# Kernel optimization log

Measured on AMD Instinct MI355X. Metric: run time of the kernel, lower is better.

The kernel has to match this reference:

```python
import jax, jax.numpy as jnp
import numpy as np

BUF = 16  # max polygon vertex buffer (convex 9-gon clipped by 4 half-planes -> <= 13 verts)


def _shoelace(V, c):
    # area of polygon stored in buffer V[:c]
    i = jnp.arange(V.shape[0])
    nxt = jnp.where(i + 1 < c, i + 1, 0)
    Vn = V[nxt]
    contrib = jnp.where(i < c, V[:, 0] * Vn[:, 1] - Vn[:, 0] * V[:, 1], 0.0)
    return 0.5 * jnp.abs(contrib.sum())


def _convex_hull(P):
    # exact convex hull of n small points; returns CCW-ordered vertex buffer [BUF,2] and count
    n = P.shape[0]
    d = P[None, :, :] - P[:, None, :]  # p_j - p_i
    minc = jnp.full((n, n), jnp.inf, P.dtype)
    for k in range(n):  # fixed small loop, keeps memory at [n,n]
        w = (P[k] - P)[:, None, :]
        minc = jnp.minimum(minc, d[..., 0] * w[..., 1] - d[..., 1] * w[..., 0])
    minc = jax.lax.stop_gradient(minc)  # hull membership is discrete
    edge = (minc >= -1e-6) & (~jnp.eye(n, dtype=bool))  # (i,j) is CCW hull edge iff all pts left
    hull = edge.any(1)
    cnt = hull.sum()
    cen = (P * hull[:, None]).sum(0) / jnp.maximum(cnt, 1)
    ang = jnp.arctan2(P[:, 1] - cen[1], P[:, 0] - cen[0])
    keyv = jnp.where(hull, jax.lax.stop_gradient(ang), jnp.inf)
    order = jnp.argsort(keyv)
    V = jnp.zeros((BUF, 2), P.dtype).at[:n].set(P[order])
    return V, cnt


def _clip(V, c, a, b):
    # Sutherland-Hodgman clip of convex polygon (V,c) by half-plane left of a->b
    i = jnp.arange(BUF)
    active = i < c
    nxt = jnp.where(i + 1 < c, i + 1, 0)
    nx = V[nxt]
    e = b - a
    s_cur = e[0] * (V[:, 1] - a[1]) - e[1] * (V[:, 0] - a[0])
    s_nxt = e[0] * (nx[:, 1] - a[1]) - e[1] * (nx[:, 0] - a[0])
    in_cur = s_cur >= 0
    in_nxt = s_nxt >= 0
    den = s_cur - s_nxt
    safe = jnp.abs(den) > 1e-9
    t = jnp.where(safe, s_cur / jnp.where(safe, den, 1.0), 0.0)
    ipt = V + t[:, None] * (nx - V)
    f_int = active & (in_cur != in_nxt)
    f_nxt = active & in_nxt
    pts = jnp.stack([ipt, nx], 1).reshape(2 * BUF, 2)
    flg = jnp.stack([f_int, f_nxt], 1).reshape(2 * BUF)
    pos = jnp.cumsum(flg) - 1
    idx = jnp.where(flg, pos, BUF)  # invalid slots dropped
    out = jnp.zeros((BUF, 2), V.dtype).at[idx].set(pts, mode='drop')
    return out, flg.sum()


def _order_ccw(Q):
    cen = Q.mean(0)
    ang = jnp.arctan2(Q[:, 1] - cen[1], Q[:, 0] - cen[0])
    return Q[jnp.argsort(jax.lax.stop_gradient(ang))]


def _per_point(gt4, p9):
    # giou_loss + out_of_box loss for one (gt quad, 9 pred points) pair
    gt = _order_ccw(gt4)
    Vp, cp = _convex_hull(p9)          # predicted convex polygon (OrientedRepPoints convex hull)
    a_pred = _shoelace(Vp, cp)
    a_gt = _shoelace(jnp.zeros((BUF, 2), gt.dtype).at[:4].set(gt), 4)
    V, c = Vp, cp
    for e in range(4):
        V, c = _clip(V, c, gt[e], gt[(e + 1) % 4])
    a_int = _shoelace(V, c)
    union = a_pred + a_gt - a_int
    iou = a_int / (union + 1e-16)
    Vh, ch = _convex_hull(jnp.concatenate([gt4, p9], 0))  # hull of all 13 points
    a_hull = _shoelace(Vh, ch)
    giou = iou - (a_hull - union) / (a_hull + 1e-16)
    # out-of-box distance: positive distance of pred points outside the gt quad edges
    b = jnp.roll(gt, -1, 0)
    e2 = b - gt
    rel = p9[:, None, :] - gt[None, :, :]
    s = (e2[None, :, 0] * rel[..., 1] - e2[None, :, 1] * rel[..., 0]) / (jnp.linalg.norm(e2, axis=1)[None, :] + 1e-9)
    oob = jax.nn.relu((-s).max(1)).mean()
    return 1.0 - giou, oob


def _assign(points_xy, points_lvl, gt_obb):
    # OBBPointAssigner: sequential per-GT closest-point assignment (pos_num=1, scale=4)
    xs = gt_obb[:, 0::2]
    ys = gt_obb[:, 1::2]
    xmin, xmax = xs.min(1), xs.max(1)
    ymin, ymax = ys.min(1), ys.max(1)
    cxy = jnp.stack([(xmin + xmax) / 2, (ymin + ymax) / 2], 1)
    wh = jnp.maximum(jnp.stack([xmax - xmin, ymax - ymin], 1), 1e-6)
    lvl_min, lvl_max = points_lvl.min(), points_lvl.max()
    glvl = jnp.clip(((jnp.log2(wh[:, 0] / 4.0) + jnp.log2(wh[:, 1] / 4.0)) / 2).astype(jnp.int32), lvl_min, lvl_max)
    K = gt_obb.shape[0]
    Np = points_xy.shape[0]

    def body(carry, g):
        inds, dist = carry
        c_xy, c_wh, c_lvl, gi = g
        dmask = points_lvl == c_lvl
        dd = jnp.linalg.norm((points_xy - c_xy) / c_wh, axis=1)
        dd = jnp.where(dmask, dd, jnp.inf)
        j = jnp.argmin(dd)
        md = dd[j]
        better = md < dist[j]
        inds = inds.at[j].set(jnp.where(better, gi + 1, inds[j]))
        dist = dist.at[j].set(jnp.where(better, md, dist[j]))
        return (inds, dist), None

    init = (jnp.zeros(Np, jnp.int32), jnp.full(Np, jnp.inf, points_xy.dtype))
    (inds, _), _ = jax.lax.scan(body, init, (cxy, wh, glvl, jnp.arange(K, dtype=jnp.int32)))
    return inds


def _stage(rep, inds, labels, gt_obb):
    posm = (labels > 0).astype(rep.dtype)
    gidx = jnp.maximum(inds - 1, 0)
    gt4 = gt_obb[gidx].reshape(-1, 4, 2)
    p9 = rep.reshape(-1, 9, 2)
    gl, oob = jax.vmap(_per_point)(gt4, p9)
    npos = jnp.maximum(posm.sum(), 1.0)
    return (gl * posm).sum() / npos, (oob * posm).sum() / npos


def _forward(rpi, rpr, cls, stride, gob, glab):
    stride = jax.lax.stop_gradient(stride)
    plvl = jnp.log2(stride).astype(jnp.int32)
    inds_i = _assign(jax.lax.stop_gradient(rpi[:, 8:10]), plvl, jax.lax.stop_gradient(gob))
    inds_r = _assign(jax.lax.stop_gradient(rpr[:, 8:10]), plvl, jax.lax.stop_gradient(gob))
    lab_i = jnp.where(inds_i > 0, glab[jnp.maximum(inds_i - 1, 0)], 0)
    lab_r = jnp.where(inds_r > 0, glab[jnp.maximum(inds_r - 1, 0)], 0)
    loc_i, sc_i = _stage(rpi, inds_i, lab_i, gob)
    loc_r, sc_r = _stage(rpr, inds_r, lab_r, gob)
    logp = jax.nn.log_softmax(cls, -1)
    cls_loss = -jnp.take_along_axis(logp, lab_r[:, None], 1).mean()
    return 1.0 * cls_loss + 0.3 * loc_i + 1.0 * loc_r + 0.05 * sc_i + 0.1 * sc_r


def setup_inputs() -> dict:
    key = jax.random.key(0)
    ks = jax.random.split(key, 8)
    strides = [8, 16, 32, 64, 128]
    batch = 2
    centers_list, stride_list = [], []
    for s in strides:
        hw = 1536 // s
        c = (jnp.arange(hw, dtype=jnp.float32) + 0.5) * s
        gx, gy = jnp.meshgrid(c, c, indexing='ij')
        cen = jnp.stack([gx.reshape(-1), gy.reshape(-1)], 1)
        cen = jnp.tile(cen, (batch, 1))
        centers_list.append(cen)
        stride_list.append(jnp.full((cen.shape[0],), float(s), jnp.float32))
    centers = jnp.concatenate(centers_list, 0)
    points_stride = jnp.concatenate(stride_list, 0)
    N = centers.shape[0]  # 98208
    base = jnp.tile(centers[:, None, :], (1, 9, 1)).reshape(N, 18)
    scale18 = jnp.repeat(points_stride[:, None], 18, 1)
    rpi = base + jax.random.normal(ks[0], (N, 18), jnp.float32) * scale18 * 1.5
    rpr = base + jax.random.normal(ks[1], (N, 18), jnp.float32) * scale18 * 1.0
    classification = jax.random.normal(ks[2], (N, 16), jnp.float32)
    K = 64
    cx = jax.random.uniform(ks[3], (K,), minval=128.0, maxval=1408.0)
    cy = jax.random.uniform(ks[4], (K,), minval=128.0, maxval=1408.0)
    w = jax.random.uniform(ks[5], (K,), minval=48.0, maxval=400.0)
    h = jax.random.uniform(ks[6], (K,), minval=48.0, maxval=400.0)
    th = jax.random.uniform(ks[7], (K,), minval=0.0, maxval=float(np.pi))
    ct, st = jnp.cos(th), jnp.sin(th)
    dx = jnp.stack([-w, w, w, -w], 1) / 2
    dy = jnp.stack([-h, -h, h, h], 1) / 2
    xs = cx[:, None] + dx * ct[:, None] - dy * st[:, None]
    ys = cy[:, None] + dx * st[:, None] + dy * ct[:, None]
    gt_obboxes = jnp.stack([xs, ys], 2).reshape(K, 8)
    gt_labels = jax.random.randint(jax.random.fold_in(key, 7), (K,), 1, 16)
    return {"rep_points_init": rpi, "rep_points_refine": rpr, "classification": classification,
            "points_stride": points_stride, "gt_obboxes": gt_obboxes, "gt_labels": gt_labels}


def reference(rep_points_init, rep_points_refine, classification, points_stride, gt_obboxes, gt_labels):
    return _forward(rep_points_init, rep_points_refine, classification, points_stride, gt_obboxes, gt_labels)
```

## Files before the change

kernel.cpp:

```cpp
#include <hip/hip_runtime.h>
#include <math.h>
#include <stdint.h>

#pragma clang fp contract(off)

#define SUB 16

struct WS {
  double sums[8];
  unsigned long long packed[128];
  int lo[8], hi[8];
  float gcx[64], gcy[64], gw[64], gh[64];
  int glvl[64];
  unsigned cntpub[2];
  unsigned done2;
};

__global__ void k_pre(const float* __restrict__ stridev, const float* __restrict__ gob,
                      int N, int K, WS* ws) {
  __shared__ int bnd[9];
  __shared__ int slmin, slmax;
  int t = threadIdx.x;
  if (t < 8) ws->sums[t] = 0.0;
  if (t < 128) ws->packed[t] = ~0ULL;
  if (t == 0) { ws->done2 = 0u; ws->cntpub[0] = 0u; ws->cntpub[1] = 0u; }
  if (t < 9) {
    float v = (float)(1 << t);
    int lo = 0, hi = N;
    while (lo < hi) { int mid = (lo + hi) >> 1; if (stridev[mid] < v) lo = mid + 1; else hi = mid; }
    bnd[t] = lo;
  }
  __syncthreads();
  if (t == 0) {
    int a = 7, b = 0;
    for (int l = 0; l < 8; l++) {
      int lo = bnd[l], hi = bnd[l + 1];
      ws->lo[l] = lo; ws->hi[l] = hi;
      if (hi > lo) { if (l < a) a = l; if (l > b) b = l; }
    }
    slmin = a; slmax = b;
  }
  __syncthreads();
  if (t < K && t < 64) {
    const float* g = gob + t * 8;
    float x0 = g[0], x1 = g[2], x2 = g[4], x3 = g[6];
    float y0 = g[1], y1 = g[3], y2 = g[5], y3 = g[7];
    float xmin = fminf(fminf(x0, x1), fminf(x2, x3));
    float xmax = fmaxf(fmaxf(x0, x1), fmaxf(x2, x3));
    float ymin = fminf(fminf(y0, y1), fminf(y2, y3));
    float ymax = fmaxf(fmaxf(y0, y1), fmaxf(y2, y3));
    float w = fmaxf(xmax - xmin, 1e-6f);
    float h = fmaxf(ymax - ymin, 1e-6f);
    ws->gcx[t] = (xmin + xmax) * 0.5f;
    ws->gcy[t] = (ymin + ymax) * 0.5f;
    ws->gw[t] = w; ws->gh[t] = h;
    int gl = (int)((log2f(w * 0.25f) + log2f(h * 0.25f)) * 0.5f);
    gl = gl < slmin ? slmin : (gl > slmax ? slmax : gl);
    ws->glvl[t] = gl;
  }
}

__global__ void __launch_bounds__(256) k_main(const float* __restrict__ rpi,
                                              const float* __restrict__ rpr,
                                              const float* __restrict__ cls,
                                              int N, int K, int AB, WS* ws) {
  __shared__ unsigned long long sb[256];
  int t = threadIdx.x;
  int b = blockIdx.x;
  if (b < AB) {
    int s = b % SUB;
    int ak = b / SUB;
    int a = ak / K;
    int k = ak % K;
    int L = ws->glvl[k];
    int lo = ws->lo[L], hi = ws->hi[L];
    float cx = ws->gcx[k], cy = ws->gcy[k], w = ws->gw[k], h = ws->gh[k];
    const float* rep = a ? rpr : rpi;
    unsigned long long best = ~0ULL;
    for (int i = lo + s * 256 + t; i < hi; i += SUB * 256) {
      const float2 p = *(const float2*)(rep + (size_t)i * 18 + 8);
      float dx = (p.x - cx) / w, dy = (p.y - cy) / h;
      float dd = sqrtf(dx * dx + dy * dy);
      unsigned long long pk = ((unsigned long long)__float_as_uint(dd) << 32) | (unsigned)i;
      if (pk < best) best = pk;
    }
    sb[t] = best;
    __syncthreads();
    for (int off = 128; off > 0; off >>= 1) {
      if (t < off) { unsigned long long o = sb[t + off]; if (o < sb[t]) sb[t] = o; }
      __syncthreads();
    }
    if (t == 0) atomicMin(&ws->packed[a * 64 + k], sb[0]);
  } else {
    int i = (b - AB) * 256 + t;
    double v = 0.0;
    if (i < N) {
      const float4* r = (const float4*)(cls + (size_t)i * 16);
      float4 q0 = r[0], q1 = r[1], q2 = r[2], q3 = r[3];
      float x[16] = {q0.x, q0.y, q0.z, q0.w, q1.x, q1.y, q1.z, q1.w,
                     q2.x, q2.y, q2.z, q2.w, q3.x, q3.y, q3.z, q3.w};
      float m = x[0];
      for (int j = 1; j < 16; j++) m = fmaxf(m, x[j]);
      float ssum = 0.f;
      for (int j = 0; j < 16; j++) ssum += expf(x[j] - m);
      v = (double)(logf(ssum) + m - x[0]);
    }
    double* sd = (double*)sb;
    sd[t] = v;
    __syncthreads();
    for (int off = 128; off > 0; off >>= 1) {
      if (t < off) sd[t] += sd[t + off];
      __syncthreads();
    }
    if (t == 0) atomicAdd(&ws->sums[0], sd[0]);
  }
}


__device__ __forceinline__ float shoe(const float* VX, const float* VY, int c) {
  float s = 0.f;
  #pragma unroll
  for (int i = 0; i < 16; i++) {
    if (i < c) {
      int nx = (i + 1 < c) ? ((i + 1 < 16) ? i + 1 : 15) : 0;
      s += VX[i] * VY[nx] - VX[nx] * VY[i];
    }
  }
  return 0.5f * fabsf(s);
}

__device__ __forceinline__ int clip_edge(const float* SX, const float* SY, float* DX, float* DY,
                                         int c, float ax, float ay, float bx, float by, int lane) {
  if (lane < 16) { DX[lane] = 0.f; DY[lane] = 0.f; }
  bool f_int = false, f_nxt = false;
  float ix = 0.f, iy = 0.f, nxv = 0.f, nyv = 0.f;
  if (lane < 16 && lane < c) {
    int nxt = (lane + 1 < c) ? lane + 1 : 0;
    if (nxt > 15) nxt = 15;
    float cxv = SX[lane], cyv = SY[lane];
    nxv = SX[nxt]; nyv = SY[nxt];
    float ex = bx - ax, ey = by - ay;
    float s_cur = ex * (cyv - ay) - ey * (cxv - ax);
    float s_nxt = ex * (nyv - ay) - ey * (nxv - ax);
    bool in_cur = s_cur >= 0.f, in_nxt = s_nxt >= 0.f;
    float den = s_cur - s_nxt;
    bool safe = fabsf(den) > 1e-9f;
    float tt = safe ? s_cur / den : 0.f;
    ix = cxv + tt * (nxv - cxv);
    iy = cyv + tt * (nyv - cyv);
    f_int = (in_cur != in_nxt);
    f_nxt = in_nxt;
  }
  unsigned long long bi = __ballot(f_int), bn = __ballot(f_nxt);
  unsigned long long lt = (1ULL << lane) - 1ULL;
  int below = __popcll(bi & lt) + __popcll(bn & lt);
  if (f_int && below < 16) { DX[below] = ix; DY[below] = iy; }
  int posn = below + (f_int ? 1 : 0);
  if (f_nxt && posn < 16) { DX[posn] = nxv; DY[posn] = nyv; }
  __syncthreads();
  return __popcll(bi) + __popcll(bn);
}

template <int NP>
__device__ __forceinline__ int hull_wave(const float* PX, const float* PY, int base,
                                         float* VX, float* VY, float* KEY, int lane) {
  constexpr int TOT = NP * NP;
  unsigned long long B0 = 0, B1 = 0, B2 = 0;
  {
    bool h = false;
    int idx = lane;
    if (idx < TOT) {
      int i = idx / NP, j = idx % NP;
      if (i != j) {
        float pix = PX[base + i], piy = PY[base + i];
        float dx = PX[base + j] - pix, dy = PY[base + j] - piy;
        float m = INFINITY;
        #pragma unroll
        for (int k = 0; k < NP; k++)
          m = fminf(m, dx * (PY[base + k] - piy) - dy * (PX[base + k] - pix));
        h = (m >= -1e-6f);
      }
    }
    B0 = __ballot(h);
  }
  if constexpr (TOT > 64) {
    bool h = false;
    int idx = lane + 64;
    if (idx < TOT) {
      int i = idx / NP, j = idx % NP;
      if (i != j) {
        float pix = PX[base + i], piy = PY[base + i];
        float dx = PX[base + j] - pix, dy = PY[base + j] - piy;
        float m = INFINITY;
        #pragma unroll
        for (int k = 0; k < NP; k++)
          m = fminf(m, dx * (PY[base + k] - piy) - dy * (PX[base + k] - pix));
        h = (m >= -1e-6f);
      }
    }
    B1 = __ballot(h);
  }
  if constexpr (TOT > 128) {
    bool h = false;
    int idx = lane + 128;
    if (idx < TOT) {
      int i = idx / NP, j = idx % NP;
      if (i != j) {
        float pix = PX[base + i], piy = PY[base + i];
        float dx = PX[base + j] - pix, dy = PY[base + j] - piy;
        float m = INFINITY;
        #pragma unroll
        for (int k = 0; k < NP; k++)
          m = fminf(m, dx * (PY[base + k] - piy) - dy * (PX[base + k] - pix));
        h = (m >= -1e-6f);
      }
    }
    B2 = __ballot(h);
  }
  bool hull_i = false;
  if (lane < NP) {
    int s = lane * NP, w = s >> 6, off = s & 63;
    unsigned long long Bw = (w == 0) ? B0 : ((w == 1) ? B1 : B2);
    unsigned long long Bw1 = (w == 0) ? B1 : ((w == 1) ? B2 : 0ULL);
    unsigned long long bits = Bw >> off;
    if (off) bits |= Bw1 << (64 - off);
    hull_i = (bits & ((1ULL << NP) - 1ULL)) != 0ULL;
  }
  unsigned long long hmask = __ballot(hull_i);
  int cnt = __popcll(hmask);
  float cx = 0.f, cy = 0.f;
  #pragma unroll
  for (int k = 0; k < NP; k++)
    if ((hmask >> k) & 1ULL) { cx += PX[base + k]; cy += PY[base + k]; }
  float dn = (float)(cnt > 1 ? cnt : 1);
  cx /= dn; cy /= dn;
  if (lane < NP)
    KEY[lane] = hull_i ? atan2f(PY[base + lane] - cy, PX[base + lane] - cx) : INFINITY;
  if (lane < 16) { VX[lane] = 0.f; VY[lane] = 0.f; }
  __syncthreads();
  if (lane < NP) {
    float ki = KEY[lane];
    int r = 0;
    #pragma unroll
    for (int j2 = 0; j2 < NP; j2++) {
      float kj = KEY[j2];
      r += (int)((kj < ki) || (kj == ki && j2 < lane));
    }
    VX[r] = PX[base + lane];
    VY[r] = PY[base + lane];
  }
  __syncthreads();
  return cnt;
}

__global__ void __launch_bounds__(64) k_post(const float* __restrict__ rpi,
                                             const float* __restrict__ rpr,
                                             const float* __restrict__ gob,
                                             const int* __restrict__ glab,
                                             const float* __restrict__ cls,
                                             int N, float* out, WS* ws) {
  __shared__ float PXs[16], PYs[16], VX[16], VY[16], DX[16], DY[16], KEY[16], RED[9];
  __shared__ int SJ[64];
  __shared__ unsigned long long SMK[64];
  int lane = threadIdx.x;
  int b = blockIdx.x;
  int a = b >> 6, p = b & 63;

  unsigned long long pk = ws->packed[a * 64 + lane];
  bool valid = (pk != ~0ULL);
  SJ[lane] = valid ? (int)(unsigned)(pk & 0xffffffffu) : (-1 - lane);
  SMK[lane] = (pk & 0xffffffff00000000ULL) | (unsigned)lane;
  __syncthreads();
  bool win = false;
  if (valid) {
    int j = SJ[lane];
    unsigned long long me = SMK[lane];
    win = true;
    for (int o = 0; o < 64; o++)
      if (SJ[o] == j && SMK[o] < me) win = false;
  }
  unsigned long long wmask = __ballot(win);
  int cnt = __popcll(wmask);
  if (p == 0 && lane == 0) atomicExch(&ws->cntpub[a], (unsigned)cnt);

  bool active = (p < cnt);
  if (active) {
    int kk = 0;
    { int c2 = 0;
      for (int o = 0; o < 64; o++)
        if ((wmask >> o) & 1ULL) { if (c2 == p) { kk = o; break; } c2++; } }
    int j = SJ[kk];
    const float* rep = (a ? rpr : rpi) + (size_t)j * 18;
    const float* gt8 = gob + (size_t)kk * 8;
    if (lane < 4) { PXs[lane] = gt8[2 * lane]; PYs[lane] = gt8[2 * lane + 1]; }
    else if (lane < 13) { int q = lane - 4; PXs[lane] = rep[2 * q]; PYs[lane] = rep[2 * q + 1]; }
    __syncthreads();

    float cenx = (((PXs[0] + PXs[1]) + PXs[2]) + PXs[3]) / 4.f;
    float ceny = (((PYs[0] + PYs[1]) + PYs[2]) + PYs[3]) / 4.f;
    float angv[4];
    int r4[4];
    #pragma unroll
    for (int i = 0; i < 4; i++) angv[i] = atan2f(PYs[i] - ceny, PXs[i] - cenx);
    #pragma unroll
    for (int i = 0; i < 4; i++) {
      int r = 0;
      #pragma unroll
      for (int j2 = 0; j2 < 4; j2++)
        r += (int)((angv[j2] < angv[i]) || (angv[j2] == angv[i] && j2 < i));
      r4[i] = r;
    }
    float qx[4], qy[4];
    #pragma unroll
    for (int d = 0; d < 4; d++) {
      float sx = 0.f, sy = 0.f;
      #pragma unroll
      for (int i = 0; i < 4; i++) if (r4[i] == d) { sx = PXs[i]; sy = PYs[i]; }
      qx[d] = sx; qy[d] = sy;
    }

    int cp = hull_wave<9>(PXs, PYs, 4, VX, VY, KEY, lane);
    float a_pred = shoe(VX, VY, cp);

    float sgt = 0.f;
    #pragma unroll
    for (int i = 0; i < 4; i++) {
      int nx = (i + 1) & 3;
      sgt += qx[i] * qy[nx] - qx[nx] * qy[i];
    }
    float a_gt = 0.5f * fabsf(sgt);

    int c = cp;
    c = clip_edge(VX, VY, DX, DY, c, qx[0], qy[0], qx[1], qy[1], lane);
    c = clip_edge(DX, DY, VX, VY, c, qx[1], qy[1], qx[2], qy[2], lane);
    c = clip_edge(VX, VY, DX, DY, c, qx[2], qy[2], qx[3], qy[3], lane);
    c = clip_edge(DX, DY, VX, VY, c, qx[3], qy[3], qx[0], qy[0], lane);
    float a_int = shoe(VX, VY, c);

    float uni = a_pred + a_gt - a_int;
    float iou = a_int / (uni + 1e-16f);

    int ch = hull_wave<13>(PXs, PYs, 0, VX, VY, KEY, lane);
    float a_hull = shoe(VX, VY, ch);
    float giou = iou - (a_hull - uni) / (a_hull + 1e-16f);
    float gl = 1.f - giou;

    float mxv = -INFINITY;
    if (lane < 36) {
      int pp = lane >> 2, e = lane & 3;
      float ax = e == 0 ? qx[0] : e == 1 ? qx[1] : e == 2 ? qx[2] : qx[3];
      float ay = e == 0 ? qy[0] : e == 1 ? qy[1] : e == 2 ? qy[2] : qy[3];
      float bx2 = e == 0 ? qx[1] : e == 1 ? qx[2] : e == 2 ? qx[3] : qx[0];
      float by2 = e == 0 ? qy[1] : e == 1 ? qy[2] : e == 2 ? qy[3] : qy[0];
      float ex = bx2 - ax, ey = by2 - ay;
      float nrm = sqrtf(ex * ex + ey * ey) + 1e-9f;
      float px = PXs[4 + pp], py = PYs[4 + pp];
      float s = (ex * (py - ay) - ey * (px - ax)) / nrm;
      mxv = -s;
    }
    float o1 = __shfl_xor(mxv, 1); mxv = fmaxf(mxv, o1);
    float o2 = __shfl_xor(mxv, 2); mxv = fmaxf(mxv, o2);
    if (lane < 36 && (lane & 3) == 0) RED[lane >> 2] = fmaxf(mxv, 0.f);
    __syncthreads();
    if (lane == 0) {
      float acc = 0.f;
      #pragma unroll
      for (int pp = 0; pp < 9; pp++) acc += RED[pp];
      float oob = acc / 9.f;
      atomicAdd(&ws->sums[1 + a * 2], (double)gl);
      atomicAdd(&ws->sums[2 + a * 2], (double)oob);
      if (a == 1) {
        int lab = glab[kk];
        double corr = (double)cls[(size_t)j * 16] - (double)cls[(size_t)j * 16 + lab];
        atomicAdd(&ws->sums[0], corr);
      }
    }
  }

  __syncthreads();
  if (lane == 0) {
    __threadfence();
    unsigned d = atomicAdd(&ws->done2, 1u);
    if (d == gridDim.x - 1) {
      __threadfence();
      double s0 = atomicAdd(&ws->sums[0], 0.0);
      double s1 = atomicAdd(&ws->sums[1], 0.0);
      double s2 = atomicAdd(&ws->sums[2], 0.0);
      double s3 = atomicAdd(&ws->sums[3], 0.0);
      double s4 = atomicAdd(&ws->sums[4], 0.0);
      unsigned c0 = atomicAdd(&ws->cntpub[0], 0u);
      unsigned c1 = atomicAdd(&ws->cntpub[1], 0u);
      double n0 = (double)(c0 > 1u ? c0 : 1u);
      double n1 = (double)(c1 > 1u ? c1 : 1u);
      out[0] = (float)(s0 / (double)N + 0.3 * (s1 / n0) + 1.0 * (s3 / n1) +
                       0.05 * (s2 / n0) + 0.1 * (s4 / n1));
    }
  }
}

extern "C" void kernel_launch(void* const* d_in, const int* in_sizes, int n_in,
                              void* d_out, int out_size, void* d_ws, size_t ws_size,
                              hipStream_t stream) {
  const float* rpi = (const float*)d_in[0];
  const float* rpr = (const float*)d_in[1];
  const float* cls = (const float*)d_in[2];
  const float* pstride = (const float*)d_in[3];
  const float* gob = (const float*)d_in[4];
  const int* glab = (const int*)d_in[5];
  int N = in_sizes[3];
  int K = in_sizes[5];
  if (K > 64) K = 64;
  WS* ws = (WS*)d_ws;

  int AB = 2 * K * SUB;
  int nb = (N + 255) / 256;
  k_pre<<<1, 256, 0, stream>>>(pstride, gob, N, K, ws);
  k_main<<<AB + nb, 256, 0, stream>>>(rpi, rpr, cls, N, K, AB, ws);
  k_post<<<128, 64, 0, stream>>>(rpi, rpr, gob, glab, cls, N, (float*)d_out, ws);
}
```

Measured before the change: 107.2 us.

## Compact rep-point coordinates into workspace and move softmax loss into pre-kernel

The pre-kernel becomes a multi-block pass that copies the center (x,y) of each rep point into a contiguous float2 array in the workspace and computes per-block cross-entropy partial sums. Level boundaries are now found with a parallel scan over exponent bits instead of binary search. The nearest-point kernel reads the compacted array, so each block touches 8 bytes per point instead of strided 72-byte rows. The last post block sums the class partials instead of using many double atomics. The cost is an extra full pass writing the compact arrays and a deterministic partial-sum buffer.

After: 203.6 us. 1.9x slower.

```diff
diff --git a/kernel.cpp b/kernel.cpp
--- a/kernel.cpp
+++ b/kernel.cpp
@@ -14,106 +14,130 @@
   int glvl[64];
   unsigned cntpub[2];
   unsigned done2;
+  unsigned pad0;
+  double clsPart[1024];
 };
 
-__global__ void k_pre(const float* __restrict__ stridev, const float* __restrict__ gob,
-                      int N, int K, WS* ws) {
-  __shared__ int bnd[9];
+__device__ __forceinline__ int lvl_of(float s) {
+  return (int)(__float_as_uint(s) >> 23) - 127;
+}
+
+__global__ void __launch_bounds__(256) k_pre(const float* __restrict__ rpi,
+                                             const float* __restrict__ rpr,
+                                             const float* __restrict__ cls,
+                                             const float* __restrict__ stridev,
+                                             const float* __restrict__ gob,
+                                             int N, int K, WS* ws) {
+  __shared__ double sd[256];
   __shared__ int slmin, slmax;
   int t = threadIdx.x;
-  if (t < 8) ws->sums[t] = 0.0;
-  if (t < 128) ws->packed[t] = ~0ULL;
-  if (t == 0) { ws->done2 = 0u; ws->cntpub[0] = 0u; ws->cntpub[1] = 0u; }
-  if (t < 9) {
-    float v = (float)(1 << t);
-    int lo = 0, hi = N;
-    while (lo < hi) { int mid = (lo + hi) >> 1; if (stridev[mid] < v) lo = mid + 1; else hi = mid; }
-    bnd[t] = lo;
-  }
-  __syncthreads();
-  if (t == 0) {
-    int a = 7, b = 0;
-    for (int l = 0; l < 8; l++) {
-      int lo = bnd[l], hi = bnd[l + 1];
-      ws->lo[l] = lo; ws->hi[l] = hi;
-      if (hi > lo) { if (l < a) a = l; if (l > b) b = l; }
-    }
-    slmin = a; slmax = b;
-  }
-  __syncthreads();
-  if (t < K && t < 64) {
-    const float* g = gob + t * 8;
-    float x0 = g[0], x1 = g[2], x2 = g[4], x3 = g[6];
-    float y0 = g[1], y1 = g[3], y2 = g[5], y3 = g[7];
-    float xmin = fminf(fminf(x0, x1), fminf(x2, x3));
-    float xmax = fmaxf(fmaxf(x0, x1), fmaxf(x2, x3));
-    float ymin = fminf(fminf(y0, y1), fminf(y2, y3));
-    float ymax = fmaxf(fmaxf(y0, y1), fmaxf(y2, y3));
-    float w = fmaxf(xmax - xmin, 1e-6f);
-    float h = fmaxf(ymax - ymin, 1e-6f);
-    ws->gcx[t] = (xmin + xmax) * 0.5f;
-    ws->gcy[t] = (ymin + ymax) * 0.5f;
-    ws->gw[t] = w; ws->gh[t] = h;
-    int gl = (int)((log2f(w * 0.25f) + log2f(h * 0.25f)) * 0.5f);
-    gl = gl < slmin ? slmin : (gl > slmax ? slmax : gl);
-    ws->glvl[t] = gl;
-  }
-}
-
-__global__ void __launch_bounds__(256) k_main(const float* __restrict__ rpi,
-                                              const float* __restrict__ rpr,
-                                              const float* __restrict__ cls,
-                                              int N, int K, int AB, WS* ws) {
+  float2* xyi = (float2*)(ws + 1);
+  float2* xyr = xyi + N;
+
+  if (blockIdx.x == 0) {
+    if (t < 8) { ws->sums[t] = 0.0; ws->lo[t] = 0; ws->hi[t] = 0; }
+    if (t < 128) ws->packed[t] = ~0ULL;
+    if (t == 0) { ws->done2 = 0u; ws->cntpub[0] = 0u; ws->cntpub[1] = 0u; }
+    __syncthreads();
+    int chunk = (N + 255) >> 8;
+    int beg = t * chunk, end = beg + chunk;
+    if (end > N) end = N;
+    if (beg < N) {
+      float prev = (beg > 0) ? stridev[beg - 1] : 0.f;
+      for (int i = beg; i < end; i++) {
+        float s = stridev[i];
+        int l = lvl_of(s);
+        if ((unsigned)l < 8u) {
+          if (i == 0) {
+            ws->lo[l] = 0;
+          } else {
+            int lp = lvl_of(prev);
+            if (lp != l) { if ((unsigned)lp < 8u) ws->hi[lp] = i; ws->lo[l] = i; }
+          }
+          if (i == N - 1) ws->hi[l] = N;
+        }
+        prev = s;
+      }
+    }
+    __syncthreads();
+    if (t == 0) {
+      int a = 7, b = 0;
+      for (int l = 0; l < 8; l++)
+        if (ws->hi[l] > ws->lo[l]) { if (l < a) a = l; if (l > b) b = l; }
+      slmin = a; slmax = b;
+    }
+    __syncthreads();
+    if (t < K && t < 64) {
+      const float* g = gob + t * 8;
+      float x0 = g[0], x1 = g[2], x2 = g[4], x3 = g[6];
+      float y0 = g[1], y1 = g[3], y2 = g[5], y3 = g[7];
+      float xmin = fminf(fminf(x0, x1), fminf(x2, x3));
+      float xmax = fmaxf(fmaxf(x0, x1), fmaxf(x2, x3));
+      float ymin = fminf(fminf(y0, y1), fminf(y2, y3));
+      float ymax = fmaxf(fmaxf(y0, y1), fmaxf(y2, y3));
+      float w = fmaxf(xmax - xmin, 1e-6f);
+      float h = fmaxf(ymax - ymin, 1e-6f);
+      ws->gcx[t] = (xmin + xmax) * 0.5f;
+      ws->gcy[t] = (ymin + ymax) * 0.5f;
+      ws->gw[t] = w; ws->gh[t] = h;
+      int gl = (int)((log2f(w * 0.25f) + log2f(h * 0.25f)) * 0.5f);
+      gl = gl < slmin ? slmin : (gl > slmax ? slmax : gl);
+      ws->glvl[t] = gl;
+    }
+  }
+
+  double acc = 0.0;
+  for (int i = blockIdx.x * 256 + t; i < N; i += gridDim.x * 256) {
+    const float* pi = rpi + (size_t)i * 18;
+    const float* pr = rpr + (size_t)i * 18;
+    xyi[i] = *(const float2*)(pi + 8);
+    xyr[i] = *(const float2*)(pr + 8);
+    const float4* r = (const float4*)(cls + (size_t)i * 16);
+    float4 q0 = r[0], q1 = r[1], q2 = r[2], q3 = r[3];
+    float x[16] = {q0.x, q0.y, q0.z, q0.w, q1.x, q1.y, q1.z, q1.w,
+                   q2.x, q2.y, q2.z, q2.w, q3.x, q3.y, q3.z, q3.w};
+    float m = x[0];
+    for (int j = 1; j < 16; j++) m = fmaxf(m, x[j]);
+    float ssum = 0.f;
+    for (int j = 0; j < 16; j++) ssum += expf(x[j] - m);
+    acc += (double)(logf(ssum) + m - x[0]);
+  }
+  sd[t] = acc;
+  __syncthreads();
+  for (int off = 128; off > 0; off >>= 1) {
+    if (t < off) sd[t] += sd[t + off];
+    __syncthreads();
+  }
+  if (t == 0) ws->clsPart[blockIdx.x] = sd[0];
+}
+
+__global__ void __launch_bounds__(256) k_main(int N, int K, WS* ws) {
   __shared__ unsigned long long sb[256];
   int t = threadIdx.x;
   int b = blockIdx.x;
-  if (b < AB) {
-    int s = b % SUB;
-    int ak = b / SUB;
-    int a = ak / K;
-    int k = ak % K;
-    int L = ws->glvl[k];
-    int lo = ws->lo[L], hi = ws->hi[L];
-    float cx = ws->gcx[k], cy = ws->gcy[k], w = ws->gw[k], h = ws->gh[k];
-    const float* rep = a ? rpr : rpi;
-    unsigned long long best = ~0ULL;
-    for (int i = lo + s * 256 + t; i < hi; i += SUB * 256) {
-      const float2 p = *(const float2*)(rep + (size_t)i * 18 + 8);
-      float dx = (p.x - cx) / w, dy = (p.y - cy) / h;
-      float dd = sqrtf(dx * dx + dy * dy);
-      unsigned long long pk = ((unsigned long long)__float_as_uint(dd) << 32) | (unsigned)i;
-      if (pk < best) best = pk;
-    }
-    sb[t] = best;
-    __syncthreads();
-    for (int off = 128; off > 0; off >>= 1) {
-      if (t < off) { unsigned long long o = sb[t + off]; if (o < sb[t]) sb[t] = o; }
-      __syncthreads();
-    }
-    if (t == 0) atomicMin(&ws->packed[a * 64 + k], sb[0]);
-  } else {
-    int i = (b - AB) * 256 + t;
-    double v = 0.0;
-    if (i < N) {
-      const float4* r = (const float4*)(cls + (size_t)i * 16);
-      float4 q0 = r[0], q1 = r[1], q2 = r[2], q3 = r[3];
-      float x[16] = {q0.x, q0.y, q0.z, q0.w, q1.x, q1.y, q1.z, q1.w,
-                     q2.x, q2.y, q2.z, q2.w, q3.x, q3.y, q3.z, q3.w};
-      float m = x[0];
-      for (int j = 1; j < 16; j++) m = fmaxf(m, x[j]);
-      float ssum = 0.f;
-      for (int j = 0; j < 16; j++) ssum += expf(x[j] - m);
-      v = (double)(logf(ssum) + m - x[0]);
-    }
-    double* sd = (double*)sb;
-    sd[t] = v;
-    __syncthreads();
-    for (int off = 128; off > 0; off >>= 1) {
-      if (t < off) sd[t] += sd[t + off];
-      __syncthreads();
-    }
-    if (t == 0) atomicAdd(&ws->sums[0], sd[0]);
-  }
+  int s = b % SUB;
+  int ak = b / SUB;
+  int a = ak / K;
+  int k = ak % K;
+  int L = ws->glvl[k];
+  int lo = ws->lo[L], hi = ws->hi[L];
+  float cx = ws->gcx[k], cy = ws->gcy[k], w = ws->gw[k], h = ws->gh[k];
+  const float2* xy = (const float2*)(ws + 1) + (a ? N : 0);
+  unsigned long long best = ~0ULL;
+  for (int i = lo + s * 256 + t; i < hi; i += SUB * 256) {
+    float2 p = xy[i];
+    float dx = (p.x - cx) / w, dy = (p.y - cy) / h;
+    float dd = sqrtf(dx * dx + dy * dy);
+    unsigned long long pk = ((unsigned long long)__float_as_uint(dd) << 32) | (unsigned)i;
+    if (pk < best) best = pk;
+  }
+  sb[t] = best;
+  __syncthreads();
+  for (int off = 128; off > 0; off >>= 1) {
+    if (t < off) { unsigned long long o = sb[t + off]; if (o < sb[t]) sb[t] = o; }
+    __syncthreads();
+  }
+  if (t == 0 && sb[0] != ~0ULL) atomicMin(&ws->packed[a * 64 + k], sb[0]);
 }
 
 
@@ -258,10 +282,12 @@
                                              const float* __restrict__ gob,
                                              const int* __restrict__ glab,
                                              const float* __restrict__ cls,
-                                             int N, float* out, WS* ws) {
+                                             int N, int nbCls, float* out, WS* ws) {
   __shared__ float PXs[16], PYs[16], VX[16], VY[16], DX[16], DY[16], KEY[16], RED[9];
   __shared__ int SJ[64];
   __shared__ unsigned long long SMK[64];
+  __shared__ double SRED[64];
+  __shared__ int islast;
   int lane = threadIdx.x;
   int b = blockIdx.x;
   int a = b >> 6, p = b & 63;
@@ -381,9 +407,19 @@
   if (lane == 0) {
     __threadfence();
     unsigned d = atomicAdd(&ws->done2, 1u);
-    if (d == gridDim.x - 1) {
-      __threadfence();
-      double s0 = atomicAdd(&ws->sums[0], 0.0);
+    islast = (d == gridDim.x - 1) ? 1 : 0;
+  }
+  __syncthreads();
+  if (islast) {
+    __threadfence();
+    double sc = 0.0;
+    for (int j = lane; j < nbCls; j += 64) sc += ws->clsPart[j];
+    SRED[lane] = sc;
+    __syncthreads();
+    if (lane == 0) {
+      double scls = 0.0;
+      for (int j = 0; j < 64; j++) scls += SRED[j];
+      double s0 = atomicAdd(&ws->sums[0], 0.0) + scls;
       double s1 = atomicAdd(&ws->sums[1], 0.0);
       double s2 = atomicAdd(&ws->sums[2], 0.0);
       double s3 = atomicAdd(&ws->sums[3], 0.0);
@@ -414,7 +450,9 @@
 
   int AB = 2 * K * SUB;
   int nb = (N + 255) / 256;
-  k_pre<<<1, 256, 0, stream>>>(pstride, gob, N, K, ws);
-  k_main<<<AB + nb, 256, 0, stream>>>(rpi, rpr, cls, N, K, AB, ws);
-  k_post<<<128, 64, 0, stream>>>(rpi, rpr, gob, glab, cls, N, (float*)d_out, ws);
-}
+  if (nb > 1024) nb = 1024;
+  if (nb < 1) nb = 1;
+  k_pre<<<nb, 256, 0, stream>>>(rpi, rpr, cls, pstride, gob, N, K, ws);
+  k_main<<<AB, 256, 0, stream>>>(N, K, ws);
+  k_post<<<128, 64, 0, stream>>>(rpi, rpr, gob, glab, cls, N, nb, (float*)d_out, ws);
+}
```
